# Kernel optimization log

Hardware: AMD Instinct MI355X
Metric: run time of the kernel (lower is better)

The kernel has to match this reference:

```python
import jax, jax.numpy as jnp
import numpy as np

W0, W1, W2 = 1.0, 1e-4, 1e-5  # loss_weight


def _gray_mask(imgs):
    """Emulate ToPILImage -> convert('L') -> mean-threshold point() -> ToTensor.
    imgs: [B,3,H,W] float in [0,1]. Returns binary mask in {0,1}, broadcast to [B,3,H,W].
    """
    u8 = jnp.floor(imgs * 255.0)  # ToPILImage: mul(255).byte() truncation
    # PIL L-mode: (R*299 + G*587 + B*114) / 1000, integer truncated
    gray = jnp.floor((u8[:, 0] * 299.0 + u8[:, 1] * 587.0 + u8[:, 2] * 114.0) / 1000.0)
    thres = gray.mean(axis=(1, 2), keepdims=True)  # np.array(mask).mean() per sample
    mask = jnp.where(gray > thres, 0.0, 1.0)       # point(0 if x>thres else 255) then /255
    return jnp.broadcast_to(mask[:, None], imgs.shape)


def _gradient_map(x):
    # finite-difference gradient magnitude with zero-padded shifts
    B, C, H, W = x.shape
    r = jnp.pad(x, ((0, 0), (0, 0), (0, 0), (0, 1)))[..., 1:]       # x[j+1], 0 at right edge
    l = jnp.pad(x, ((0, 0), (0, 0), (0, 0), (1, 0)))[..., :W]       # x[j-1], 0 at left edge
    t = jnp.pad(x, ((0, 0), (0, 0), (1, 0), (0, 0)))[..., :H, :]    # x[i-1], 0 at top edge
    b = jnp.pad(x, ((0, 0), (0, 0), (0, 1), (0, 0)))[..., 1:, :]    # x[i+1], 0 at bottom edge
    return jnp.sqrt(((r - l) * 0.5) ** 2 + ((t - b) * 0.5) ** 2 + 1e-6)


def setup_inputs() -> dict:
    key = jax.random.key(0)
    k1, k2, k3, k4 = jax.random.split(key, 4)
    return {
        "out_images": jax.random.uniform(k1, (128, 3, 128, 512), dtype=jnp.float32),
        "target_images": jax.random.uniform(k2, (128, 3, 128, 512), dtype=jnp.float32),
        "text_pred": jax.random.normal(k3, (4096, 10000), dtype=jnp.float32),
        "text_gt": jax.random.randint(k4, (4096,), 0, 10000, dtype=jnp.int64),
    }


def reference(out_images, target_images, text_pred, text_gt):
    # l2: MSE over images
    l2 = jnp.mean((out_images - target_images) ** 2)
    # lg: L1 between gradient maps of binarized masks (masks are detached: built via PIL)
    mo = jax.lax.stop_gradient(_gray_mask(out_images))
    mt = jax.lax.stop_gradient(_gray_mask(target_images))
    lg = jnp.mean(jnp.abs(_gradient_map(mo) - _gradient_map(mt)))
    # lce: mean cross-entropy
    logp = jax.nn.log_softmax(text_pred, axis=-1)
    ce = -jnp.mean(jnp.take_along_axis(logp, text_gt[:, None], axis=-1))
    return W0 * l2 + W1 * lg + W2 * ce
```

## Files before the change

kernel.cpp:

```cpp
#include <hip/hip_runtime.h>
#include <hip/hip_bf16.h>
#include <math.h>

#define BB 128
#define HH 128
#define WW 512
#define HW (HH*WW)
#define NPIX ((size_t)BB*HW)
#define ROWS 4096
#define COLS 10000
#define P1_BLOCKS (BB*16)
#define LCE_BLOCKS 2048
#define GRID (P1_BLOCKS + LCE_BLOCKS)


__device__ __forceinline__ int gray_of(float r, float g, float b) {
    int ri = (int)floorf(r * 255.0f);
    int gi = (int)floorf(g * 255.0f);
    int bi = (int)floorf(b * 255.0f);
    return (299 * ri + 587 * gi + 114 * bi) / 1000;
}

__device__ __forceinline__ float e4(float4 x) {
    return (__expf(x.x) + __expf(x.y)) + (__expf(x.z) + __expf(x.w));
}

template <bool STORE_GRAY>
__global__ __launch_bounds__(256, 2) void fused1_kernel(
    const float* __restrict__ outI, const float* __restrict__ tgtI,
    const float* __restrict__ X, const int* __restrict__ gt,
    float* __restrict__ l2p, int* __restrict__ gso, int* __restrict__ gst,
    float* __restrict__ cesp, float* __restrict__ xgp,
    unsigned char* __restrict__ gout, unsigned char* __restrict__ gtgt) {
    const int tid = threadIdx.x;
    const int bid = blockIdx.x;
    const int wid = tid >> 6, lane = tid & 63;

    if ((bid & 1) == 0) {
        const int p1    = bid >> 1;
        const int b     = p1 >> 4;
        const int chunk = p1 & 15;
        const float4* o4 = (const float4*)(outI + (size_t)b * 3 * HW) + chunk * 1024;
        const float4* t4 = (const float4*)(tgtI + (size_t)b * 3 * HW) + chunk * 1024;
        uchar4* go4 = (uchar4*)(gout + (size_t)b * HW) + chunk * 1024;
        uchar4* gt4 = (uchar4*)(gtgt + (size_t)b * HW) + chunk * 1024;

        float4 o[12], t[12];
#pragma unroll
        for (int k = 0; k < 4; ++k) {
            int v = tid + k * 256;
            o[3*k+0] = o4[v]; o[3*k+1] = o4[v + HW/4]; o[3*k+2] = o4[v + 2*(HW/4)];
            t[3*k+0] = t4[v]; t[3*k+1] = t4[v + HW/4]; t[3*k+2] = t4[v + 2*(HW/4)];
        }
        __builtin_amdgcn_sched_barrier(0);

        float l2 = 0.0f;
        int so = 0, st = 0;
#pragma unroll
        for (int k = 0; k < 4; ++k) {
            float4 oR = o[3*k], oG = o[3*k+1], oB = o[3*k+2];
            float4 tR = t[3*k], tG = t[3*k+1], tB = t[3*k+2];
            float d;
            d = oR.x-tR.x; l2 += d*d;  d = oR.y-tR.y; l2 += d*d;
            d = oR.z-tR.z; l2 += d*d;  d = oR.w-tR.w; l2 += d*d;
            d = oG.x-tG.x; l2 += d*d;  d = oG.y-tG.y; l2 += d*d;
            d = oG.z-tG.z; l2 += d*d;  d = oG.w-tG.w; l2 += d*d;
            d = oB.x-tB.x; l2 += d*d;  d = oB.y-tB.y; l2 += d*d;
            d = oB.z-tB.z; l2 += d*d;  d = oB.w-tB.w; l2 += d*d;

            int g0 = gray_of(oR.x, oG.x, oB.x);
            int g1 = gray_of(oR.y, oG.y, oB.y);
            int g2 = gray_of(oR.z, oG.z, oB.z);
            int g3 = gray_of(oR.w, oG.w, oB.w);
            so += g0 + g1 + g2 + g3;
            if (STORE_GRAY) go4[tid + k*256] = make_uchar4((unsigned char)g0,(unsigned char)g1,(unsigned char)g2,(unsigned char)g3);
            g0 = gray_of(tR.x, tG.x, tB.x);
            g1 = gray_of(tR.y, tG.y, tB.y);
            g2 = gray_of(tR.z, tG.z, tB.z);
            g3 = gray_of(tR.w, tG.w, tB.w);
            st += g0 + g1 + g2 + g3;
            if (STORE_GRAY) gt4[tid + k*256] = make_uchar4((unsigned char)g0,(unsigned char)g1,(unsigned char)g2,(unsigned char)g3);
        }

        for (int off = 32; off > 0; off >>= 1) {
            l2 += __shfl_down(l2, off);
            so += __shfl_down(so, off);
            st += __shfl_down(st, off);
        }
        __shared__ float wl2[4];
        __shared__ int w1[4], w2[4];
        if (lane == 0) { wl2[wid] = l2; w1[wid] = so; w2[wid] = st; }
        __syncthreads();
        if (tid == 0) {
            l2p[p1] = wl2[0] + wl2[1] + wl2[2] + wl2[3];
            gso[p1] = w1[0] + w1[1] + w1[2] + w1[3];
            gst[p1] = w2[0] + w2[1] + w2[2] + w2[3];
        }
    } else {
        const int unit = (bid >> 1) * 4 + wid;
        const int row  = unit >> 1;
        const int h    = unit & 1;
        const float4* xh = (const float4*)(X + (size_t)row * COLS) + h * 1250;

        float s = 0.0f;
#pragma unroll
        for (int k = 0; k < 4; ++k) {
            int v = lane + k * 256;
            float4 a = xh[v], b2 = xh[v+64], c = xh[v+128], d = xh[v+192];
            s += e4(a) + e4(b2) + e4(c) + e4(d);
        }
        {
            float4 a = xh[1024+lane], b2 = xh[1088+lane], c = xh[1152+lane];
            s += e4(a) + e4(b2) + e4(c);
            if (1216 + lane < 1250) s += e4(xh[1216+lane]);
        }
        for (int off = 32; off > 0; off >>= 1) s += __shfl_down(s, off);
        if (lane == 0) {
            cesp[unit] = s;
            if (h == 0) xgp[row] = X[(size_t)row * COLS + gt[row]];
        }
    }
}

__device__ __forceinline__ int mask8(uint2 v, int ti) {
    int m = 0;
#pragma unroll
    for (int k = 0; k < 4; ++k) m |= (((int)((v.x >> (8*k)) & 255) <= ti) ? 1 : 0) << k;
#pragma unroll
    for (int k = 0; k < 4; ++k) m |= (((int)((v.y >> (8*k)) & 255) <= ti) ? 1 : 0) << (k+4);
    return m;
}

__device__ __forceinline__ void grad_bits(const unsigned char* __restrict__ G,
                                          int r, int roff, int ti, int lane,
                                          int& ax, int& vy) {
    uint2 cc = *(const uint2*)(G + roff);
    uint2 aa = *(const uint2*)(G + (r > 0   ? roff - 512 : roff));
    uint2 bb = *(const uint2*)(G + (r < 127 ? roff + 512 : roff));
    int mc = mask8(cc, ti);
    int ma = (r > 0)   ? mask8(aa, ti) : 0;
    int mb = (r < 127) ? mask8(bb, ti) : 0;
    int prev = __shfl_up(mc, 1);
    int next = __shfl_down(mc, 1);
    int lb = ((mc << 1) & 0xFF) | ((lane > 0)  ? ((prev >> 7) & 1) : 0);
    int rb = (mc >> 1)          | ((lane < 63) ? ((next & 1) << 7) : 0);
    ax = lb ^ rb;
    vy = ma ^ mb;
}

__global__ __launch_bounds__(256) void pass2_kernel(
    const unsigned char* __restrict__ gout, const unsigned char* __restrict__ gtgt,
    const int* __restrict__ gso, const int* __restrict__ gst,
    float* __restrict__ lgp) {
    const int tid  = threadIdx.x;
    const int wave = tid >> 6, lane = tid & 63;
    const int b  = blockIdx.x >> 4;
    const int rg = blockIdx.x & 15;

    int s_o = 0, s_t = 0;
#pragma unroll
    for (int k = 0; k < 16; ++k) { s_o += gso[b*16 + k]; s_t += gst[b*16 + k]; }
    const int ti_o = s_o >> 16;
    const int ti_t = s_t >> 16;
    const unsigned char* Go = gout + (size_t)b * HW;
    const unsigned char* Gt = gtgt + (size_t)b * HW;

    const float v0 = sqrtf(1e-6f);
    const float v1 = sqrtf(0.25f + 1e-6f);
    const float v2 = sqrtf(0.5f + 1e-6f);

    float sum = 0.0f;
#pragma unroll
    for (int rr = 0; rr < 2; ++rr) {
        const int r = rg * 8 + wave * 2 + rr;
        const int roff = r * 512 + lane * 8;
        int ax_o, vy_o, ax_t, vy_t;
        grad_bits(Go, r, roff, ti_o, lane, ax_o, vy_o);
        grad_bits(Gt, r, roff, ti_t, lane, ax_t, vy_t);
#pragma unroll
        for (int k = 0; k < 8; ++k) {
            int so = ((ax_o >> k) & 1) + ((vy_o >> k) & 1);
            int st = ((ax_t >> k) & 1) + ((vy_t >> k) & 1);
            float g_o = (so == 0) ? v0 : ((so == 1) ? v1 : v2);
            float g_t = (st == 0) ? v0 : ((st == 1) ? v1 : v2);
            sum += fabsf(g_o - g_t);
        }
    }

    for (int off = 32; off > 0; off >>= 1) sum += __shfl_down(sum, off);
    __shared__ float ws4[4];
    if (lane == 0) ws4[wave] = sum;
    __syncthreads();
    if (tid == 0) lgp[blockIdx.x] = ws4[0] + ws4[1] + ws4[2] + ws4[3];
}

__device__ __forceinline__ float mask_at(const float* __restrict__ img, size_t base, int p, float thres) {
    float r = img[base + p], g = img[base + p + HW], b = img[base + p + 2*HW];
    return ((float)gray_of(r, g, b) > thres) ? 0.0f : 1.0f;
}

__global__ __launch_bounds__(256) void pass2_recompute_kernel(
    const float* __restrict__ outI, const float* __restrict__ tgtI,
    const int* __restrict__ gso, const int* __restrict__ gst,
    float* __restrict__ lgp) {
    const int tid   = threadIdx.x;
    const int b     = blockIdx.x >> 4;
    const int chunk = blockIdx.x & 15;
    int s_o = 0, s_t = 0;
    for (int k = 0; k < 16; ++k) { s_o += gso[b*16 + k]; s_t += gst[b*16 + k]; }
    const float to = (float)s_o * (1.0f/65536.0f);
    const float tt = (float)s_t * (1.0f/65536.0f);
    const size_t baseO = (size_t)b * 3 * HW;

    float sum = 0.0f;
    for (int u = 0; u < 16; ++u) {
        int p = chunk * 4096 + u * 256 + tid;
        int i = p >> 9, j = p & 511;
        float mr = (j+1 < WW) ? mask_at(outI, baseO, p+1,  to) : 0.0f;
        float ml = (j-1 >= 0) ? mask_at(outI, baseO, p-1,  to) : 0.0f;
        float mt = (i-1 >= 0) ? mask_at(outI, baseO, p-WW, to) : 0.0f;
        float mb = (i+1 < HH) ? mask_at(outI, baseO, p+WW, to) : 0.0f;
        float dx = (mr - ml) * 0.5f, dy = (mt - mb) * 0.5f;
        float gmo = sqrtf(dx*dx + dy*dy + 1e-6f);
        mr = (j+1 < WW) ? mask_at(tgtI, baseO, p+1,  tt) : 0.0f;
        ml = (j-1 >= 0) ? mask_at(tgtI, baseO, p-1,  tt) : 0.0f;
        mt = (i-1 >= 0) ? mask_at(tgtI, baseO, p-WW, tt) : 0.0f;
        mb = (i+1 < HH) ? mask_at(tgtI, baseO, p+WW, tt) : 0.0f;
        dx = (mr - ml) * 0.5f; dy = (mt - mb) * 0.5f;
        float gmt = sqrtf(dx*dx + dy*dy + 1e-6f);
        sum += fabsf(gmo - gmt);
    }

    __shared__ float sred[256];
    sred[tid] = sum;
    __syncthreads();
    for (int off = 128; off > 0; off >>= 1) {
        if (tid < off) sred[tid] += sred[tid+off];
        __syncthreads();
    }
    if (tid == 0) lgp[blockIdx.x] = sred[0];
}

__global__ __launch_bounds__(256) void combine_kernel(
    const float* __restrict__ l2p, const float* __restrict__ lgp,
    const float* __restrict__ cesp, const float* __restrict__ xgp,
    float* __restrict__ out) {
    __shared__ double s0[256], s1[256], s2[256];
    const int t = threadIdx.x;
    double a = 0.0, bsum = 0.0, c = 0.0;
    for (int i = t; i < 2048; i += 256) { a += (double)l2p[i]; bsum += (double)lgp[i]; }
    for (int i = t; i < 4096; i += 256)
        c += (double)(__logf(cesp[2*i] + cesp[2*i+1]) - xgp[i]);
    s0[t] = a; s1[t] = bsum; s2[t] = c;
    __syncthreads();
    for (int off = 128; off > 0; off >>= 1) {
        if (t < off) { s0[t] += s0[t+off]; s1[t] += s1[t+off]; s2[t] += s2[t+off]; }
        __syncthreads();
    }
    if (t == 0) {
        double l2 = s0[0] / (double)(3.0 * (double)NPIX);
        double lg = s1[0] / (double)NPIX;
        double ce = s2[0] / (double)ROWS;
        out[0] = (float)(l2 + 1e-4 * lg + 1e-5 * ce);
    }
}

extern "C" void kernel_launch(void* const* d_in, const int* in_sizes, int n_in,
                              void* d_out, int out_size, void* d_ws, size_t ws_size,
                              hipStream_t stream) {
    const float* outI = (const float*)d_in[0];
    const float* tgtI = (const float*)d_in[1];
    const float* X    = (const float*)d_in[2];
    const int*   gt   = (const int*)d_in[3];

    float* l2p  = (float*)d_ws;
    int*   gso  = (int*)((char*)d_ws + 8192);
    int*   gst  = (int*)((char*)d_ws + 16384);
    float* lgp  = (float*)((char*)d_ws + 24576);
    float* cesp = (float*)((char*)d_ws + 32768);
    float* xgp  = (float*)((char*)d_ws + 65536);
    unsigned char* gray = (unsigned char*)d_ws + 98304;
    const size_t need = 98304 + 2 * NPIX;
    const bool useCache = ws_size >= need;

    if (useCache) {
        fused1_kernel<true><<<GRID, 256, 0, stream>>>(
            outI, tgtI, X, gt, l2p, gso, gst, cesp, xgp, gray, gray + NPIX);
        pass2_kernel<<<BB * 16, 256, 0, stream>>>(gray, gray + NPIX, gso, gst, lgp);
    } else {
        fused1_kernel<false><<<GRID, 256, 0, stream>>>(
            outI, tgtI, X, gt, l2p, gso, gst, cesp, xgp, gray, gray);
        pass2_recompute_kernel<<<BB * 16, 256, 0, stream>>>(outI, tgtI, gso, gst, lgp);
    }
    combine_kernel<<<1, 256, 0, stream>>>(l2p, lgp, cesp, xgp, (float*)d_out);
}
```

Baseline: 93.48 us.

## Stream image and logit loads through LDS with double-buffered global_load_lds

```diff
diff --git a/kernel.cpp b/kernel.cpp
--- a/kernel.cpp
+++ b/kernel.cpp
@@ -25,41 +25,58 @@
     return (__expf(x.x) + __expf(x.y)) + (__expf(x.z) + __expf(x.w));
 }
 
+__device__ __forceinline__ void gload16(const float* g, void* l) {
+    __builtin_amdgcn_global_load_lds(
+        (const __attribute__((address_space(1))) void*)g,
+        (__attribute__((address_space(3))) void*)l, 16, 0, 0);
+}
+
+#define WAITV6() do { asm volatile("s_waitcnt vmcnt(6)" ::: "memory"); \
+                      __builtin_amdgcn_sched_barrier(0); } while (0)
+#define WAITV0() do { asm volatile("s_waitcnt vmcnt(0)" ::: "memory"); \
+                      __builtin_amdgcn_sched_barrier(0); } while (0)
+
 template <bool STORE_GRAY>
-__global__ __launch_bounds__(256, 2) void fused1_kernel(
+__global__ __launch_bounds__(256) void fused1_kernel(
     const float* __restrict__ outI, const float* __restrict__ tgtI,
     const float* __restrict__ X, const int* __restrict__ gt,
     float* __restrict__ l2p, int* __restrict__ gso, int* __restrict__ gst,
     float* __restrict__ cesp, float* __restrict__ xgp,
     unsigned char* __restrict__ gout, unsigned char* __restrict__ gtgt) {
+    __shared__ __align__(16) unsigned char lds[4][2][6][1024];
     const int tid = threadIdx.x;
     const int bid = blockIdx.x;
-    const int wid = tid >> 6, lane = tid & 63;
+    const int w = tid >> 6, lane = tid & 63;
 
     if ((bid & 1) == 0) {
         const int p1    = bid >> 1;
         const int b     = p1 >> 4;
-        const int chunk = p1 & 15;
-        const float4* o4 = (const float4*)(outI + (size_t)b * 3 * HW) + chunk * 1024;
-        const float4* t4 = (const float4*)(tgtI + (size_t)b * 3 * HW) + chunk * 1024;
-        uchar4* go4 = (uchar4*)(gout + (size_t)b * HW) + chunk * 1024;
-        uchar4* gt4 = (uchar4*)(gtgt + (size_t)b * HW) + chunk * 1024;
-
-        float4 o[12], t[12];
-#pragma unroll
-        for (int k = 0; k < 4; ++k) {
-            int v = tid + k * 256;
-            o[3*k+0] = o4[v]; o[3*k+1] = o4[v + HW/4]; o[3*k+2] = o4[v + 2*(HW/4)];
-            t[3*k+0] = t4[v]; t[3*k+1] = t4[v + HW/4]; t[3*k+2] = t4[v + 2*(HW/4)];
-        }
-        __builtin_amdgcn_sched_barrier(0);
+        const int px0   = (p1 & 15) * 4096;
+        const float* baseO = outI + (size_t)b * 3 * HW + px0 + w * 1024;
+        const float* baseT = tgtI + (size_t)b * 3 * HW + px0 + w * 1024;
+        uchar4* goB = (uchar4*)(gout + (size_t)b * HW + px0 + w * 1024);
+        uchar4* gtB = (uchar4*)(gtgt + (size_t)b * HW + px0 + w * 1024);
 
         float l2 = 0.0f;
         int so = 0, st = 0;
-#pragma unroll
-        for (int k = 0; k < 4; ++k) {
-            float4 oR = o[3*k], oG = o[3*k+1], oB = o[3*k+2];
-            float4 tR = t[3*k], tG = t[3*k+1], tB = t[3*k+2];
+
+        auto issue = [&](int c, int p) {
+            const float* sO = baseO + c * 256 + lane * 4;
+            const float* sT = baseT + c * 256 + lane * 4;
+            gload16(sO,          &lds[w][p][0][0]);
+            gload16(sO + HW,     &lds[w][p][1][0]);
+            gload16(sO + 2*HW,   &lds[w][p][2][0]);
+            gload16(sT,          &lds[w][p][3][0]);
+            gload16(sT + HW,     &lds[w][p][4][0]);
+            gload16(sT + 2*HW,   &lds[w][p][5][0]);
+        };
+        auto compute = [&](int c, int p) {
+            const float4 oR = *(const float4*)&lds[w][p][0][lane*16];
+            const float4 oG = *(const float4*)&lds[w][p][1][lane*16];
+            const float4 oB = *(const float4*)&lds[w][p][2][lane*16];
+            const float4 tR = *(const float4*)&lds[w][p][3][lane*16];
+            const float4 tG = *(const float4*)&lds[w][p][4][lane*16];
+            const float4 tB = *(const float4*)&lds[w][p][5][lane*16];
             float d;
             d = oR.x-tR.x; l2 += d*d;  d = oR.y-tR.y; l2 += d*d;
             d = oR.z-tR.z; l2 += d*d;  d = oR.w-tR.w; l2 += d*d;
@@ -73,14 +90,22 @@
             int g2 = gray_of(oR.z, oG.z, oB.z);
             int g3 = gray_of(oR.w, oG.w, oB.w);
             so += g0 + g1 + g2 + g3;
-            if (STORE_GRAY) go4[tid + k*256] = make_uchar4((unsigned char)g0,(unsigned char)g1,(unsigned char)g2,(unsigned char)g3);
+            if (STORE_GRAY) goB[c*64 + lane] = make_uchar4((unsigned char)g0,(unsigned char)g1,(unsigned char)g2,(unsigned char)g3);
             g0 = gray_of(tR.x, tG.x, tB.x);
             g1 = gray_of(tR.y, tG.y, tB.y);
             g2 = gray_of(tR.z, tG.z, tB.z);
             g3 = gray_of(tR.w, tG.w, tB.w);
             st += g0 + g1 + g2 + g3;
-            if (STORE_GRAY) gt4[tid + k*256] = make_uchar4((unsigned char)g0,(unsigned char)g1,(unsigned char)g2,(unsigned char)g3);
-        }
+            if (STORE_GRAY) gtB[c*64 + lane] = make_uchar4((unsigned char)g0,(unsigned char)g1,(unsigned char)g2,(unsigned char)g3);
+        };
+
+        issue(0, 0); issue(1, 1);
+        WAITV6(); compute(0, 0);
+        issue(2, 0);
+        WAITV6(); compute(1, 1);
+        issue(3, 1);
+        WAITV6(); compute(2, 0);
+        WAITV0(); compute(3, 1);
 
         for (int off = 32; off > 0; off >>= 1) {
             l2 += __shfl_down(l2, off);
@@ -89,7 +114,7 @@
         }
         __shared__ float wl2[4];
         __shared__ int w1[4], w2[4];
-        if (lane == 0) { wl2[wid] = l2; w1[wid] = so; w2[wid] = st; }
+        if (lane == 0) { wl2[w] = l2; w1[w] = so; w2[w] = st; }
         __syncthreads();
         if (tid == 0) {
             l2p[p1] = wl2[0] + wl2[1] + wl2[2] + wl2[3];
@@ -97,23 +122,38 @@
             gst[p1] = w2[0] + w2[1] + w2[2] + w2[3];
         }
     } else {
-        const int unit = (bid >> 1) * 4 + wid;
+        const int unit = (bid >> 1) * 4 + w;
         const int row  = unit >> 1;
         const int h    = unit & 1;
-        const float4* xh = (const float4*)(X + (size_t)row * COLS) + h * 1250;
+        const float* Xh = X + (size_t)row * COLS + h * 5000;
+        const float4* xh4 = (const float4*)Xh;
 
         float s = 0.0f;
-#pragma unroll
-        for (int k = 0; k < 4; ++k) {
-            int v = lane + k * 256;
-            float4 a = xh[v], b2 = xh[v+64], c = xh[v+128], d = xh[v+192];
-            s += e4(a) + e4(b2) + e4(c) + e4(d);
-        }
         {
-            float4 a = xh[1024+lane], b2 = xh[1088+lane], c = xh[1152+lane];
-            s += e4(a) + e4(b2) + e4(c);
-            if (1216 + lane < 1250) s += e4(xh[1216+lane]);
-        }
+            float4 a = xh4[1152 + lane];
+            s += e4(a);
+            if (lane < 34) { float4 b2 = xh4[1216 + lane]; s += e4(b2); }
+        }
+
+        auto issueL = [&](int k, int p) {
+            const float* src = Xh + k * 1536 + lane * 4;
+#pragma unroll
+            for (int j = 0; j < 6; ++j) gload16(src + j * 256, &lds[w][p][j][0]);
+        };
+        auto computeL = [&](int p) {
+#pragma unroll
+            for (int j = 0; j < 6; ++j) {
+                float4 a = *(const float4*)&lds[w][p][j][lane*16];
+                s += e4(a);
+            }
+        };
+
+        issueL(0, 0); issueL(1, 1);
+        WAITV6(); computeL(0);
+        issueL(2, 0);
+        WAITV6(); computeL(1);
+        WAITV0(); computeL(0);
+
         for (int off = 32; off > 0; off >>= 1) s += __shfl_down(s, off);
         if (lane == 0) {
             cesp[unit] = s;
```

Result: slower. 95.57 us (+2.2%).

## Split LCE rows into quarter-row waves and interleave 1:2 with image blocks

Applied to the files above, without the earlier changes.

```diff
diff --git a/kernel.cpp b/kernel.cpp
--- a/kernel.cpp
+++ b/kernel.cpp
@@ -10,9 +10,11 @@
 #define ROWS 4096
 #define COLS 10000
 #define P1_BLOCKS (BB*16)
-#define LCE_BLOCKS 2048
+#define LCE_BLOCKS 4096
 #define GRID (P1_BLOCKS + LCE_BLOCKS)
 
+
+typedef float vf4 __attribute__((ext_vector_type(4)));
 
 __device__ __forceinline__ int gray_of(float r, float g, float b) {
     int ri = (int)floorf(r * 255.0f);
@@ -21,12 +23,12 @@
     return (299 * ri + 587 * gi + 114 * bi) / 1000;
 }
 
-__device__ __forceinline__ float e4(float4 x) {
+__device__ __forceinline__ float e4v(vf4 x) {
     return (__expf(x.x) + __expf(x.y)) + (__expf(x.z) + __expf(x.w));
 }
 
 template <bool STORE_GRAY>
-__global__ __launch_bounds__(256, 2) void fused1_kernel(
+__global__ __launch_bounds__(256) void fused1_kernel(
     const float* __restrict__ outI, const float* __restrict__ tgtI,
     const float* __restrict__ X, const int* __restrict__ gt,
     float* __restrict__ l2p, int* __restrict__ gso, int* __restrict__ gst,
@@ -34,10 +36,10 @@
     unsigned char* __restrict__ gout, unsigned char* __restrict__ gtgt) {
     const int tid = threadIdx.x;
     const int bid = blockIdx.x;
-    const int wid = tid >> 6, lane = tid & 63;
-
-    if ((bid & 1) == 0) {
-        const int p1    = bid >> 1;
+    const int w = tid >> 6, lane = tid & 63;
+
+    if (bid % 3 == 0) {
+        const int p1    = bid / 3;
         const int b     = p1 >> 4;
         const int chunk = p1 & 15;
         const float4* o4 = (const float4*)(outI + (size_t)b * 3 * HW) + chunk * 1024;
@@ -45,21 +47,13 @@
         uchar4* go4 = (uchar4*)(gout + (size_t)b * HW) + chunk * 1024;
         uchar4* gt4 = (uchar4*)(gtgt + (size_t)b * HW) + chunk * 1024;
 
-        float4 o[12], t[12];
+        float l2 = 0.0f;
+        int so = 0, st = 0;
 #pragma unroll
         for (int k = 0; k < 4; ++k) {
             int v = tid + k * 256;
-            o[3*k+0] = o4[v]; o[3*k+1] = o4[v + HW/4]; o[3*k+2] = o4[v + 2*(HW/4)];
-            t[3*k+0] = t4[v]; t[3*k+1] = t4[v + HW/4]; t[3*k+2] = t4[v + 2*(HW/4)];
-        }
-        __builtin_amdgcn_sched_barrier(0);
-
-        float l2 = 0.0f;
-        int so = 0, st = 0;
-#pragma unroll
-        for (int k = 0; k < 4; ++k) {
-            float4 oR = o[3*k], oG = o[3*k+1], oB = o[3*k+2];
-            float4 tR = t[3*k], tG = t[3*k+1], tB = t[3*k+2];
+            float4 oR = o4[v], oG = o4[v + HW/4], oB = o4[v + 2*(HW/4)];
+            float4 tR = t4[v], tG = t4[v + HW/4], tB = t4[v + 2*(HW/4)];
             float d;
             d = oR.x-tR.x; l2 += d*d;  d = oR.y-tR.y; l2 += d*d;
             d = oR.z-tR.z; l2 += d*d;  d = oR.w-tR.w; l2 += d*d;
@@ -73,13 +67,13 @@
             int g2 = gray_of(oR.z, oG.z, oB.z);
             int g3 = gray_of(oR.w, oG.w, oB.w);
             so += g0 + g1 + g2 + g3;
-            if (STORE_GRAY) go4[tid + k*256] = make_uchar4((unsigned char)g0,(unsigned char)g1,(unsigned char)g2,(unsigned char)g3);
+            if (STORE_GRAY) go4[v] = make_uchar4((unsigned char)g0,(unsigned char)g1,(unsigned char)g2,(unsigned char)g3);
             g0 = gray_of(tR.x, tG.x, tB.x);
             g1 = gray_of(tR.y, tG.y, tB.y);
             g2 = gray_of(tR.z, tG.z, tB.z);
             g3 = gray_of(tR.w, tG.w, tB.w);
             st += g0 + g1 + g2 + g3;
-            if (STORE_GRAY) gt4[tid + k*256] = make_uchar4((unsigned char)g0,(unsigned char)g1,(unsigned char)g2,(unsigned char)g3);
+            if (STORE_GRAY) gt4[v] = make_uchar4((unsigned char)g0,(unsigned char)g1,(unsigned char)g2,(unsigned char)g3);
         }
 
         for (int off = 32; off > 0; off >>= 1) {
@@ -89,7 +83,7 @@
         }
         __shared__ float wl2[4];
         __shared__ int w1[4], w2[4];
-        if (lane == 0) { wl2[wid] = l2; w1[wid] = so; w2[wid] = st; }
+        if (lane == 0) { wl2[w] = l2; w1[w] = so; w2[w] = st; }
         __syncthreads();
         if (tid == 0) {
             l2p[p1] = wl2[0] + wl2[1] + wl2[2] + wl2[3];
@@ -97,27 +91,26 @@
             gst[p1] = w2[0] + w2[1] + w2[2] + w2[3];
         }
     } else {
-        const int unit = (bid >> 1) * 4 + wid;
-        const int row  = unit >> 1;
-        const int h    = unit & 1;
-        const float4* xh = (const float4*)(X + (size_t)row * COLS) + h * 1250;
+        const int lceb = (bid / 3) * 2 + (bid % 3 - 1);
+        const int unit = lceb * 4 + w;
+        const int row  = unit >> 2;
+        const int q    = unit & 3;
+        const vf4* xq4 = (const vf4*)(X + (size_t)row * COLS + q * 2500);
 
         float s = 0.0f;
 #pragma unroll
-        for (int k = 0; k < 4; ++k) {
-            int v = lane + k * 256;
-            float4 a = xh[v], b2 = xh[v+64], c = xh[v+128], d = xh[v+192];
-            s += e4(a) + e4(b2) + e4(c) + e4(d);
-        }
-        {
-            float4 a = xh[1024+lane], b2 = xh[1088+lane], c = xh[1152+lane];
-            s += e4(a) + e4(b2) + e4(c);
-            if (1216 + lane < 1250) s += e4(xh[1216+lane]);
+        for (int k = 0; k < 9; ++k) {
+            vf4 a = __builtin_nontemporal_load(xq4 + lane + k * 64);
+            s += e4v(a);
+        }
+        if (lane < 49) {
+            vf4 a = __builtin_nontemporal_load(xq4 + 576 + lane);
+            s += e4v(a);
         }
         for (int off = 32; off > 0; off >>= 1) s += __shfl_down(s, off);
         if (lane == 0) {
             cesp[unit] = s;
-            if (h == 0) xgp[row] = X[(size_t)row * COLS + gt[row]];
+            if (q == 0) xgp[row] = X[(size_t)row * COLS + gt[row]];
         }
     }
 }
@@ -249,8 +242,10 @@
     const int t = threadIdx.x;
     double a = 0.0, bsum = 0.0, c = 0.0;
     for (int i = t; i < 2048; i += 256) { a += (double)l2p[i]; bsum += (double)lgp[i]; }
-    for (int i = t; i < 4096; i += 256)
-        c += (double)(__logf(cesp[2*i] + cesp[2*i+1]) - xgp[i]);
+    for (int i = t; i < 4096; i += 256) {
+        float s = (cesp[4*i] + cesp[4*i+1]) + (cesp[4*i+2] + cesp[4*i+3]);
+        c += (double)(__logf(s) - xgp[i]);
+    }
     s0[t] = a; s1[t] = bsum; s2[t] = c;
     __syncthreads();
     for (int off = 128; off > 0; off >>= 1) {
@@ -278,9 +273,9 @@
     int*   gst  = (int*)((char*)d_ws + 16384);
     float* lgp  = (float*)((char*)d_ws + 24576);
     float* cesp = (float*)((char*)d_ws + 32768);
-    float* xgp  = (float*)((char*)d_ws + 65536);
-    unsigned char* gray = (unsigned char*)d_ws + 98304;
-    const size_t need = 98304 + 2 * NPIX;
+    float* xgp  = (float*)((char*)d_ws + 98304);
+    unsigned char* gray = (unsigned char*)d_ws + 131072;
+    const size_t need = 131072 + 2 * NPIX;
     const bool useCache = ws_size >= need;
 
     if (useCache) {
```

After: 82.05 us. -12.2%, faster.
